# Optimization experiments

Hardware: AMD Instinct MI355X
Metric: run time of the kernel (lower is better)

## Reference

```python
import jax, jax.numpy as jnp
import numpy as np

B, L, LO, H, V = 8, 1024, 1024, 768, 4096
NUM_TAGS = 256


def _merge_one(tags):
    """Replicates merge_weights() for one sequence of tags [L].

    A maximal run of equal, non-(-1) tags becomes one output row that averages
    the hidden states over the run. A run is only emitted when it is *closed*
    by a tag change or a -1 (so a run ending at the last position is dropped,
    exactly like the torch loop). Remaining rows are zero with bias -100.
    """
    Ls = tags.shape[0]
    pos = jnp.arange(Ls)
    valid = tags != -1
    prev = jnp.concatenate([jnp.full((1,), -2, tags.dtype), tags[:-1]])
    start = valid & ((pos == 0) | (tags != prev) | (prev == -1))
    seg_id = jnp.cumsum(start.astype(jnp.int32)) - 1          # run index per position
    total_runs = seg_id[-1] + 1
    emitted = total_runs - valid[-1].astype(jnp.int32)        # trailing open run dropped
    seg_clip = jnp.clip(seg_id, 0, Ls - 1)
    # run lengths via segment sum (invalid positions contribute 0)
    counts = jax.ops.segment_sum(valid.astype(jnp.float32), seg_clip, num_segments=Ls)
    w = jnp.where(valid & (seg_id >= 0) & (seg_id < emitted),
                  1.0 / jnp.maximum(counts[seg_clip], 1.0), 0.0)
    merge = jnp.zeros((Ls, Ls), jnp.float32).at[seg_clip, pos].add(w)  # [rows, tokens]
    bias = jnp.where(pos < emitted, 0.0, -100.0)
    return merge, bias


def setup_inputs() -> dict:
    key = jax.random.key(0)
    k1, k2, k3, k4 = jax.random.split(key, 4)
    hidden1_states = jax.random.normal(k1, (B, L, H), jnp.float32)
    hidden2_states = jax.random.normal(k2, (B, LO, H), jnp.float32)
    lm_logits = jax.random.normal(k3, (B, LO, V), jnp.float32)
    tags = jnp.sort(jax.random.randint(k4, (B, L), 0, NUM_TAGS), axis=-1)
    return {"hidden1_states": hidden1_states, "hidden2_states": hidden2_states,
            "lm_logits": lm_logits, "tags": tags}


def reference(hidden1_states, hidden2_states, lm_logits, tags):
    merge, bias = jax.vmap(_merge_one)(tags)                     # [B,L,L], [B,L]
    attn = jnp.einsum('bls,bsh->blh', merge, hidden1_states)     # segment means
    attn1 = jnp.einsum('boh,blh->bol', hidden2_states, attn) + bias[:, None, :]
    return jnp.concatenate([lm_logits, attn1], axis=2)           # [B,LO,V+L]
```

## Files before the change

### kernel.cpp

```cpp
#include <hip/hip_runtime.h>
#include <hip/hip_bf16.h>
#include <stdint.h>

#define BB   8
#define LL   1024
#define LOO  1024
#define HH   768
#define VV   4096
#define OUTW 5120
#define EMAX 256

typedef unsigned short ushort_t;
typedef __attribute__((ext_vector_type(4))) float   f32x4;
typedef __attribute__((ext_vector_type(8))) __bf16  bf16x8;
typedef __attribute__((ext_vector_type(4))) float   float4v;
typedef __attribute__((ext_vector_type(4))) unsigned short ushort4v;

static __device__ __forceinline__ ushort_t f2bf(float f) {
    union { float f; uint32_t u; } v; v.f = f;
    uint32_t u = v.u;
    uint32_t r = (u + 0x7fffu + ((u >> 16) & 1u)) >> 16;
    return (ushort_t)r;
}

__global__ void seg_kernel(const int* __restrict__ tags,
                           int* __restrict__ seg_start,
                           int* __restrict__ emitted) {
    int b = blockIdx.x;
    int p = threadIdx.x;
    const int* t = tags + b * LL;
    int myTag = t[p];
    int isStart = (p == 0) || (myTag != t[p - 1]);
    __shared__ int sc[LL];
    sc[p] = isStart;
    __syncthreads();
    for (int off = 1; off < LL; off <<= 1) {
        int v   = sc[p];
        int add = (p >= off) ? sc[p - off] : 0;
        __syncthreads();
        sc[p] = v + add;
        __syncthreads();
    }
    int incl = sc[p];
    if (isStart) seg_start[b * (LL + 1) + (incl - 1)] = p;
    if (p == LL - 1) {
        emitted[b] = incl - 1;
        seg_start[b * (LL + 1) + incl] = LL;
    }
}

__global__ void attn_kernel(const float* __restrict__ h1,
                            const int* __restrict__ seg_start,
                            const int* __restrict__ emitted,
                            ushort_t* __restrict__ attn) {
    int b = blockIdx.x >> 8;
    int r = blockIdx.x & 255;
    int em = emitted[b];
    ushort_t* arow = attn + ((size_t)b * EMAX + r) * HH;
    int tid = threadIdx.x;
    if (r >= em) {
        arow[tid] = 0; arow[tid + 256] = 0; arow[tid + 512] = 0;
        return;
    }
    const int* ss = seg_start + b * (LL + 1);
    int s = ss[r], e = ss[r + 1];
    float inv = 1.0f / (float)(e - s);
    const float* hb = h1 + (size_t)b * LL * HH;
    float a0 = 0.f, a1 = 0.f, a2 = 0.f;
    for (int p = s; p < e; ++p) {
        const float* row = hb + (size_t)p * HH;
        a0 += row[tid]; a1 += row[tid + 256]; a2 += row[tid + 512];
    }
    arow[tid]       = f2bf(a0 * inv);
    arow[tid + 256] = f2bf(a1 * inv);
    arow[tid + 512] = f2bf(a2 * inv);
}

__global__ void cast_h2_kernel(const float* __restrict__ h2,
                               ushort_t* __restrict__ h2b) {
    int i = blockIdx.x * blockDim.x + threadIdx.x;
    float4v v = ((const float4v*)h2)[i];
    ushort4v o;
    o[0] = f2bf(v[0]); o[1] = f2bf(v[1]); o[2] = f2bf(v[2]); o[3] = f2bf(v[3]);
    ((ushort4v*)h2b)[i] = o;
}

#define NGEMM 128
#define NCOPY 2048
__global__ __launch_bounds__(256, 2) void mega_kernel(
        const ushort_t* __restrict__ A,
        const ushort_t* __restrict__ Bm,
        const int* __restrict__ emitted,
        const float* __restrict__ lm,
        float* __restrict__ out) {
    __shared__ char smem[32768];

    if (blockIdx.x >= NGEMM) {
        int cid = blockIdx.x - NGEMM;
        int tid = threadIdx.x;
        const float4v* in4 = (const float4v*)lm;
        float4v* out4 = (float4v*)out;
        int c = cid * 256 + tid;
#pragma unroll
        for (int g = 0; g < 4; ++g) {
            size_t i0 = (size_t)(g * 4 + 0) * 524288 + c;
            size_t i1 = (size_t)(g * 4 + 1) * 524288 + c;
            size_t i2 = (size_t)(g * 4 + 2) * 524288 + c;
            size_t i3 = (size_t)(g * 4 + 3) * 524288 + c;
            float4v v0 = in4[i0];
            float4v v1 = in4[i1];
            float4v v2 = in4[i2];
            float4v v3 = in4[i3];
            out4[i0 + ((i0 >> 10) << 8)] = v0;
            out4[i1 + ((i1 >> 10) << 8)] = v1;
            out4[i2 + ((i2 >> 10) << 8)] = v2;
            out4[i3 + ((i3 >> 10) << 8)] = v3;
        }
        float4v fv = {-100.f, -100.f, -100.f, -100.f};
        if (tid < 192) {
#pragma unroll
            for (int j = 0; j < 4; ++j) {
                size_t row = (size_t)cid * 4 + j;
                out4[row * (OUTW / 4) + (VV + 256) / 4 + tid] = fv;
            }
        }
        return;
    }

    int bid  = blockIdx.x;
    int b    = bid >> 4;
    int t2   = bid & 15;
    int brow = (t2 >> 1) << 7;
    int bcol = (t2 & 1) << 7;

    const int tid  = threadIdx.x;
    const int lane = tid & 63;
    const int wid  = tid >> 6;
    const int wr   = (wid >> 1) & 1;
    const int wc   = wid & 1;

    const ushort_t* Ab = A  + (size_t)b * LOO * HH;
    const ushort_t* Bb = Bm + (size_t)b * EMAX * HH;

    f32x4 zero = {0.f, 0.f, 0.f, 0.f};
    f32x4 acc[4][4];
#pragma unroll
    for (int i = 0; i < 4; ++i)
#pragma unroll
        for (int j = 0; j < 4; ++j) acc[i][j] = zero;

    for (int k0 = 0; k0 < HH; k0 += 64) {
        __syncthreads();
#pragma unroll
        for (int i = 0; i < 4; ++i) {
            int off = i * 4096 + tid * 16;
            int row = off >> 7;
            int cb  = off & 127;
            int scb = cb ^ ((row & 7) << 4);
            const ushort_t* ga = Ab + (size_t)(brow + row) * HH + k0 + (scb >> 1);
            const ushort_t* gb = Bb + (size_t)(bcol + row) * HH + k0 + (scb >> 1);
            __builtin_amdgcn_global_load_lds(
                (const __attribute__((address_space(1))) void*)ga,
                (__attribute__((address_space(3))) void*)(smem + off), 16, 0, 0);
            __builtin_amdgcn_global_load_lds(
                (const __attribute__((address_space(1))) void*)gb,
                (__attribute__((address_space(3))) void*)(smem + 16384 + off), 16, 0, 0);
        }
        asm volatile("s_waitcnt vmcnt(0)" ::: "memory");
        __syncthreads();

#pragma unroll
        for (int ks = 0; ks < 2; ++ks) {
            bf16x8 af[4], bfr[4];
#pragma unroll
            for (int mi = 0; mi < 4; ++mi) {
                int row  = (wr << 6) + (mi << 4) + (lane & 15);
                int colb = (ks << 6) + ((lane >> 4) << 4);
                int addr = (row << 7) + (colb ^ ((row & 7) << 4));
                af[mi] = *(const bf16x8*)(smem + addr);
            }
#pragma unroll
            for (int ni = 0; ni < 4; ++ni) {
                int row  = (wc << 6) + (ni << 4) + (lane & 15);
                int colb = (ks << 6) + ((lane >> 4) << 4);
                int addr = (row << 7) + (colb ^ ((row & 7) << 4));
                bfr[ni] = *(const bf16x8*)(smem + 16384 + addr);
            }
#pragma unroll
            for (int mi = 0; mi < 4; ++mi)
#pragma unroll
                for (int ni = 0; ni < 4; ++ni)
                    acc[mi][ni] = __builtin_amdgcn_mfma_f32_16x16x32_bf16(
                        af[mi], bfr[ni], acc[mi][ni], 0, 0, 0);
        }
    }

    int em = emitted[b];
    float* outb = out + (size_t)b * LOO * OUTW + VV;
#pragma unroll
    for (int mi = 0; mi < 4; ++mi) {
        int rbase = brow + (wr << 6) + (mi << 4) + ((lane >> 4) << 2);
#pragma unroll
        for (int ni = 0; ni < 4; ++ni) {
            int col = bcol + (wc << 6) + (ni << 4) + (lane & 15);
            float badd = (col < em) ? 0.0f : -100.0f;
#pragma unroll
            for (int rr = 0; rr < 4; ++rr)
                outb[(size_t)(rbase + rr) * OUTW + col] = acc[mi][ni][rr] + badd;
        }
    }
}

extern "C" void kernel_launch(void* const* d_in, const int* in_sizes, int n_in,
                              void* d_out, int out_size, void* d_ws, size_t ws_size,
                              hipStream_t stream) {
    const float* h1   = (const float*)d_in[0];
    const float* h2   = (const float*)d_in[1];
    const float* lm   = (const float*)d_in[2];
    const int*   tags = (const int*)d_in[3];
    float* out = (float*)d_out;

    char* ws = (char*)d_ws;
    ushort_t* h2b      = (ushort_t*)ws;
    ushort_t* attn     = (ushort_t*)(ws + 12582912);
    int*      seg_strt = (int*)(ws + 12582912 + 3145728);
    int*      emitted  = (int*)(ws + 12582912 + 3145728 + 32800);

    seg_kernel<<<BB, LL, 0, stream>>>(tags, seg_strt, emitted);
    attn_kernel<<<BB * EMAX, 256, 0, stream>>>(h1, seg_strt, emitted, attn);
    cast_h2_kernel<<<(BB * LOO * HH / 4) / 256, 256, 0, stream>>>(h2, h2b);
    mega_kernel<<<NGEMM + NCOPY, 256, 0, stream>>>(h2b, attn, emitted, lm, out);
}
```

Baseline: 95.38 us.

## Fuse segment scan into attn kernel and cast h2 to bf16 inside GEMM

Removes the separate segment-scan kernel: each attn block now recomputes the run starts for its batch from the tags in shared memory. Removes the h2 cast kernel: the GEMM loads fp32 h2 tiles straight into LDS through a larger swizzled buffer and converts them to bf16 in registers before the MFMAs. This cuts two launches and a 12MB write plus reread of bf16 h2. In exchange it adds redundant scan work in every attn block, doubles the A-tile load bytes, and enlarges LDS, which may lower occupancy.

```diff
diff --git a/kernel.cpp b/kernel.cpp
--- a/kernel.cpp
+++ b/kernel.cpp
@@ -14,7 +14,7 @@
 typedef __attribute__((ext_vector_type(4))) float   f32x4;
 typedef __attribute__((ext_vector_type(8))) __bf16  bf16x8;
 typedef __attribute__((ext_vector_type(4))) float   float4v;
-typedef __attribute__((ext_vector_type(4))) unsigned short ushort4v;
+typedef __attribute__((ext_vector_type(4))) int     int4v;
 
 static __device__ __forceinline__ ushort_t f2bf(float f) {
     union { float f; uint32_t u; } v; v.f = f;
@@ -23,47 +23,56 @@
     return (ushort_t)r;
 }
 
-__global__ void seg_kernel(const int* __restrict__ tags,
-                           int* __restrict__ seg_start,
-                           int* __restrict__ emitted) {
-    int b = blockIdx.x;
-    int p = threadIdx.x;
-    const int* t = tags + b * LL;
-    int myTag = t[p];
-    int isStart = (p == 0) || (myTag != t[p - 1]);
-    __shared__ int sc[LL];
-    sc[p] = isStart;
-    __syncthreads();
-    for (int off = 1; off < LL; off <<= 1) {
-        int v   = sc[p];
-        int add = (p >= off) ? sc[p - off] : 0;
-        __syncthreads();
-        sc[p] = v + add;
-        __syncthreads();
-    }
-    int incl = sc[p];
-    if (isStart) seg_start[b * (LL + 1) + (incl - 1)] = p;
-    if (p == LL - 1) {
-        emitted[b] = incl - 1;
-        seg_start[b * (LL + 1) + incl] = LL;
-    }
-}
-
-__global__ void attn_kernel(const float* __restrict__ h1,
-                            const int* __restrict__ seg_start,
-                            const int* __restrict__ emitted,
-                            ushort_t* __restrict__ attn) {
+__global__ __launch_bounds__(256) void attn_fused_kernel(
+        const float* __restrict__ h1,
+        const int* __restrict__ tags,
+        ushort_t* __restrict__ attn,
+        int* __restrict__ emitted_out) {
     int b = blockIdx.x >> 8;
     int r = blockIdx.x & 255;
-    int em = emitted[b];
+    int tid = threadIdx.x;
+
+    __shared__ int stags[LL];
+    __shared__ int cnt[256];
+    __shared__ int runpos[EMAX + 2];
+
+    ((int4v*)stags)[tid] = ((const int4v*)(tags + b * LL))[tid];
+    __syncthreads();
+
+    int p0 = tid * 4;
+    int st[4];
+    int prevm1 = (p0 == 0) ? -2 : stags[p0 - 1];
+    st[0] = (p0 == 0) || (stags[p0] != prevm1);
+    st[1] = (stags[p0 + 1] != stags[p0]);
+    st[2] = (stags[p0 + 2] != stags[p0 + 1]);
+    st[3] = (stags[p0 + 3] != stags[p0 + 2]);
+    int c = st[0] + st[1] + st[2] + st[3];
+    cnt[tid] = c;
+    __syncthreads();
+    for (int off = 1; off < 256; off <<= 1) {
+        int v = cnt[tid];
+        int a = (tid >= off) ? cnt[tid - off] : 0;
+        __syncthreads();
+        cnt[tid] = v + a;
+        __syncthreads();
+    }
+    int total = cnt[255];
+    int base = cnt[tid] - c;
+#pragma unroll
+    for (int j = 0; j < 4; ++j)
+        if (st[j]) runpos[base++] = p0 + j;
+    if (tid == 0) runpos[total] = LL;
+    __syncthreads();
+
+    int em = total - 1;
+    if (r == 0 && tid == 0) emitted_out[b] = em;
+
     ushort_t* arow = attn + ((size_t)b * EMAX + r) * HH;
-    int tid = threadIdx.x;
     if (r >= em) {
         arow[tid] = 0; arow[tid + 256] = 0; arow[tid + 512] = 0;
         return;
     }
-    const int* ss = seg_start + b * (LL + 1);
-    int s = ss[r], e = ss[r + 1];
+    int s = runpos[r], e = runpos[r + 1];
     float inv = 1.0f / (float)(e - s);
     const float* hb = h1 + (size_t)b * LL * HH;
     float a0 = 0.f, a1 = 0.f, a2 = 0.f;
@@ -76,24 +85,15 @@
     arow[tid + 512] = f2bf(a2 * inv);
 }
 
-__global__ void cast_h2_kernel(const float* __restrict__ h2,
-                               ushort_t* __restrict__ h2b) {
-    int i = blockIdx.x * blockDim.x + threadIdx.x;
-    float4v v = ((const float4v*)h2)[i];
-    ushort4v o;
-    o[0] = f2bf(v[0]); o[1] = f2bf(v[1]); o[2] = f2bf(v[2]); o[3] = f2bf(v[3]);
-    ((ushort4v*)h2b)[i] = o;
-}
-
 #define NGEMM 128
 #define NCOPY 2048
 __global__ __launch_bounds__(256, 2) void mega_kernel(
-        const ushort_t* __restrict__ A,
+        const float* __restrict__ A,
         const ushort_t* __restrict__ Bm,
         const int* __restrict__ emitted,
         const float* __restrict__ lm,
         float* __restrict__ out) {
-    __shared__ char smem[32768];
+    __shared__ char smem[49152];
 
     if (blockIdx.x >= NGEMM) {
         int cid = blockIdx.x - NGEMM;
@@ -139,7 +139,7 @@
     const int wr   = (wid >> 1) & 1;
     const int wc   = wid & 1;
 
-    const ushort_t* Ab = A  + (size_t)b * LOO * HH;
+    const float*    Ab = A  + (size_t)b * LOO * HH;
     const ushort_t* Bb = Bm + (size_t)b * EMAX * HH;
 
     f32x4 zero = {0.f, 0.f, 0.f, 0.f};
@@ -151,20 +151,27 @@
 
     for (int k0 = 0; k0 < HH; k0 += 64) {
         __syncthreads();
+#pragma unroll
+        for (int i = 0; i < 8; ++i) {
+            int off = i * 4096 + tid * 16;
+            int row = off >> 8;
+            int cb  = off & 255;
+            int scb = cb ^ ((row & 7) << 5);
+            const float* ga = Ab + (size_t)(brow + row) * HH + k0 + (scb >> 2);
+            __builtin_amdgcn_global_load_lds(
+                (const __attribute__((address_space(1))) void*)ga,
+                (__attribute__((address_space(3))) void*)(smem + off), 16, 0, 0);
+        }
 #pragma unroll
         for (int i = 0; i < 4; ++i) {
             int off = i * 4096 + tid * 16;
             int row = off >> 7;
             int cb  = off & 127;
             int scb = cb ^ ((row & 7) << 4);
-            const ushort_t* ga = Ab + (size_t)(brow + row) * HH + k0 + (scb >> 1);
             const ushort_t* gb = Bb + (size_t)(bcol + row) * HH + k0 + (scb >> 1);
             __builtin_amdgcn_global_load_lds(
-                (const __attribute__((address_space(1))) void*)ga,
-                (__attribute__((address_space(3))) void*)(smem + off), 16, 0, 0);
-            __builtin_amdgcn_global_load_lds(
                 (const __attribute__((address_space(1))) void*)gb,
-                (__attribute__((address_space(3))) void*)(smem + 16384 + off), 16, 0, 0);
+                (__attribute__((address_space(3))) void*)(smem + 32768 + off), 16, 0, 0);
         }
         asm volatile("s_waitcnt vmcnt(0)" ::: "memory");
         __syncthreads();
@@ -175,16 +182,23 @@
 #pragma unroll
             for (int mi = 0; mi < 4; ++mi) {
                 int row  = (wr << 6) + (mi << 4) + (lane & 15);
-                int colb = (ks << 6) + ((lane >> 4) << 4);
-                int addr = (row << 7) + (colb ^ ((row & 7) << 4));
-                af[mi] = *(const bf16x8*)(smem + addr);
+                int colb = (ks << 7) + ((lane >> 4) << 5);
+                int addr = (row << 8) + (colb ^ ((row & 7) << 5));
+                f32x4 a0 = *(const f32x4*)(smem + addr);
+                f32x4 a1 = *(const f32x4*)(smem + addr + 16);
+                bf16x8 t;
+                t[0] = (__bf16)a0[0]; t[1] = (__bf16)a0[1];
+                t[2] = (__bf16)a0[2]; t[3] = (__bf16)a0[3];
+                t[4] = (__bf16)a1[0]; t[5] = (__bf16)a1[1];
+                t[6] = (__bf16)a1[2]; t[7] = (__bf16)a1[3];
+                af[mi] = t;
             }
 #pragma unroll
             for (int ni = 0; ni < 4; ++ni) {
                 int row  = (wc << 6) + (ni << 4) + (lane & 15);
                 int colb = (ks << 6) + ((lane >> 4) << 4);
                 int addr = (row << 7) + (colb ^ ((row & 7) << 4));
-                bfr[ni] = *(const bf16x8*)(smem + 16384 + addr);
+                bfr[ni] = *(const bf16x8*)(smem + 32768 + addr);
             }
 #pragma unroll
             for (int mi = 0; mi < 4; ++mi)
@@ -221,13 +235,9 @@
     float* out = (float*)d_out;
 
     char* ws = (char*)d_ws;
-    ushort_t* h2b      = (ushort_t*)ws;
-    ushort_t* attn     = (ushort_t*)(ws + 12582912);
-    int*      seg_strt = (int*)(ws + 12582912 + 3145728);
-    int*      emitted  = (int*)(ws + 12582912 + 3145728 + 32800);
-
-    seg_kernel<<<BB, LL, 0, stream>>>(tags, seg_strt, emitted);
-    attn_kernel<<<BB * EMAX, 256, 0, stream>>>(h1, seg_strt, emitted, attn);
-    cast_h2_kernel<<<(BB * LOO * HH / 4) / 256, 256, 0, stream>>>(h2, h2b);
-    mega_kernel<<<NGEMM + NCOPY, 256, 0, stream>>>(h2b, attn, emitted, lm, out);
-}
+    ushort_t* attn    = (ushort_t*)ws;
+    int*      emitted = (int*)(ws + 3145728);
+
+    attn_fused_kernel<<<BB * EMAX, 256, 0, stream>>>(h1, tags, attn, emitted);
+    mega_kernel<<<NGEMM + NCOPY, 256, 0, stream>>>(h2, attn, emitted, lm, out);
+}
```

New measurement: 85.08 us. -10.8%, faster.
